# Performance work log

Hardware: AMD Instinct MI355X
Metric: run time of the kernel (lower is better)

The kernel has to match this reference:

```python
import jax, jax.numpy as jnp
import numpy as np

N_NODES = 20000
N_EDGES = 320000
N_ADJ = 4
D = 256
CSTR = [0, 1]          # constrained adjacency subset for the last step
RATIO = 1.0
LN_EPS = 1e-5


def setup_inputs() -> dict:
    key = jax.random.key(0)
    ks = jax.random.split(key, 10)
    x = jax.random.normal(ks[0], (N_NODES, D), dtype=jnp.float32)
    rows = jax.random.randint(ks[1], (N_ADJ, N_EDGES), 0, N_NODES)
    cols = jax.random.randint(ks[2], (N_ADJ, N_EDGES), 0, N_NODES)
    vals = jax.random.uniform(ks[3], (N_ADJ, N_EDGES), dtype=jnp.float32)
    W = jax.random.normal(ks[4], (D, D), dtype=jnp.float32) * (1.0 / np.sqrt(D))
    b = jax.random.normal(ks[5], (D,), dtype=jnp.float32) * 0.02
    ws_seq_0 = jax.random.uniform(ks[6], (2, N_ADJ - 1), dtype=jnp.float32)
    ws_seq_1 = jax.random.uniform(ks[7], (len(CSTR),), dtype=jnp.float32)
    ws_res_0 = jax.random.uniform(ks[8], (1, N_ADJ), dtype=jnp.float32)
    ws_res_1 = jax.random.uniform(ks[9], (2, len(CSTR) + 1), dtype=jnp.float32)
    return {"x": x, "rows": rows, "cols": cols, "vals": vals, "W": W, "b": b,
            "ws_seq_0": ws_seq_0, "ws_seq_1": ws_seq_1,
            "ws_res_0": ws_res_0, "ws_res_1": ws_res_1}


def reference(x, rows, cols, vals, W, b, ws_seq_0, ws_seq_1, ws_res_0, ws_res_1):
    n_nodes = x.shape[0]

    def spmm(a, h):
        # sparse [n,n] @ h : gather source features, scale, scatter-add by row
        return jax.ops.segment_sum(vals[a][:, None] * h[cols[a]], rows[a],
                                   num_segments=n_nodes)

    def op(h, adj_ids, w):
        # Op with k=1: random.sample selects ALL operators -> weighted mean
        acc = w[0] * spmm(adj_ids[0], h)
        for j, a in enumerate(adj_ids[1:], start=1):
            acc = acc + w[j] * spmm(a, h)
        return acc / len(adj_ids)

    h = x @ W + b                      # affine: [n_nodes, D]
    states = [h]
    # step i=0: seq only (res sum over states[:0] is empty -> 0), edge == 1
    s1 = op(states[0], [0, 1, 2], ws_seq_0[0])          # adjs[:-1]
    states.append(s1)
    # step i=1: seq on states[1] over adjs[:-1], res on states[0] over all adjs
    s2 = op(states[1], [0, 1, 2], ws_seq_0[1]) + RATIO * op(states[0], [0, 1, 2, 3], ws_res_0[0])
    states.append(s2)
    # last step: cstr adjacencies for seq; cstr + last adj for residuals
    out_seq = op(states[2], CSTR, ws_seq_1)
    res_ids = CSTR + [N_ADJ - 1]
    out_res = op(states[0], res_ids, ws_res_1[0]) + op(states[1], res_ids, ws_res_1[1])
    out = out_seq + RATIO * out_res
    # LayerNorm without affine params
    mu = jnp.mean(out, axis=-1, keepdims=True)
    var = jnp.var(out, axis=-1, keepdims=True)
    out = (out - mu) * jax.lax.rsqrt(var + LN_EPS)
    return jax.nn.gelu(out, approximate=False)
```

## Files before the change

### kernel.cpp

```cpp
#include <hip/hip_runtime.h>
#include <hip/hip_bf16.h>

#define N_NODES 20000
#define N_EDGES 320000
#define N_ADJ   4
#define D       256
#define DH      128
#define RPA     20004

#define NBUCK   79
#define NGRP    40
#define EPB     8000
#define GCAP    192
#define BMAX    4736
#define MMBLK   1250

typedef __attribute__((ext_vector_type(8))) short bf8;
typedef __attribute__((ext_vector_type(4))) float f4;


__device__ __forceinline__ unsigned f2bf_bits(float x) {
    unsigned u = __float_as_uint(x);
    return (u + 0x7FFFu + ((u >> 16) & 1u)) >> 16;
}
__device__ __forceinline__ unsigned pack_bf2(float lo, float hi) {
    return f2bf_bits(lo) | (f2bf_bits(hi) << 16);
}
__device__ __forceinline__ float bf_lo(unsigned p) { return __uint_as_float(p << 16); }
__device__ __forceinline__ float bf_hi(unsigned p) { return __uint_as_float(p & 0xFFFF0000u); }


__global__ __launch_bounds__(1024) void prep_kernel(const int* __restrict__ rows,
                                                    const int* __restrict__ cols,
                                                    const float* __restrict__ vals,
                                                    int* __restrict__ cnt,
                                                    uint2* __restrict__ stage,
                                                    const float* __restrict__ W,
                                                    uint4* __restrict__ wh,
                                                    uint4* __restrict__ wl) {
    __shared__ int lcnt[NBUCK];
    int g = blockIdx.x, a = blockIdx.y, t = threadIdx.x;

    if (g >= NGRP) {
        if (a != 0) return;
        for (int i = (g - NGRP) * 1024 + t; i < 8192; i += 2048) {
            int lane = i & 63;
            int tile = i >> 6;
            int ks = tile >> 4, n = tile & 15;
            int m = lane & 15, quad = lane >> 4;
            int col = n * 16 + m;
            int k0  = ks * 32 + quad * 8;
            unsigned hbits[8], lbits[8];
            #pragma unroll
            for (int j = 0; j < 8; ++j) {
                float v = W[(k0 + j) * D + col];
                unsigned hb = f2bf_bits(v);
                float lo = v - __uint_as_float(hb << 16);
                hbits[j] = hb;
                lbits[j] = f2bf_bits(lo);
            }
            uint4 hh, ll;
            hh.x = hbits[0] | (hbits[1] << 16); hh.y = hbits[2] | (hbits[3] << 16);
            hh.z = hbits[4] | (hbits[5] << 16); hh.w = hbits[6] | (hbits[7] << 16);
            ll.x = lbits[0] | (lbits[1] << 16); ll.y = lbits[2] | (lbits[3] << 16);
            ll.z = lbits[4] | (lbits[5] << 16); ll.w = lbits[6] | (lbits[7] << 16);
            wh[i] = hh;
            wl[i] = ll;
        }
        return;
    }

    if (t < NBUCK) lcnt[t] = 0;
    __syncthreads();
    int e0 = g * EPB;
    #pragma unroll 1
    for (int i = 0; i < EPB; i += 1024) {
        int e = e0 + i + t;
        if (i + t < EPB) {
            int r   = rows[a * N_EDGES + e];
            int c   = cols[a * N_EDGES + e];
            float v = vals[a * N_EDGES + e];
            int b   = r >> 8;
            int idx = atomicAdd(&lcnt[b], 1);
            if (idx < GCAP) {
                stage[(size_t)((a * NBUCK + b) * NGRP + g) * GCAP + idx] =
                    make_uint2((f2bf_bits(v) << 16) | (unsigned)c, (unsigned)(r & 255));
            }
        }
    }
    __syncthreads();
    if (t < NBUCK) cnt[(a * NBUCK + t) * NGRP + g] = min(lcnt[t], GCAP);
}


__global__ __launch_bounds__(256) void mm_kernel(const float* __restrict__ x,
                                                 const uint4* __restrict__ wh,
                                                 const uint4* __restrict__ wl,
                                                 const float* __restrict__ bvec,
                                                 unsigned* __restrict__ hp) {
    int t = threadIdx.x;
    int wid = t >> 6, lane = t & 63;
    int r0 = blockIdx.x * 16;
    int m = lane & 15, quad = lane >> 4;

    const float* xr = x + (size_t)(r0 + m) * D + quad * 8;
    bf8 ah[8], al[8];
    #pragma unroll
    for (int ks = 0; ks < 8; ++ks) {
        float4 v0 = *(const float4*)(xr + ks * 32);
        float4 v1 = *(const float4*)(xr + ks * 32 + 4);
        float xs[8] = {v0.x, v0.y, v0.z, v0.w, v1.x, v1.y, v1.z, v1.w};
        #pragma unroll
        for (int j = 0; j < 8; ++j) {
            unsigned hb = f2bf_bits(xs[j]);
            float lo = xs[j] - __uint_as_float(hb << 16);
            ah[ks][j] = (short)hb;
            al[ks][j] = (short)f2bf_bits(lo);
        }
    }

    #pragma unroll
    for (int i = 0; i < 4; ++i) {
        int n = wid * 4 + i;
        f4 c = {0.f, 0.f, 0.f, 0.f};
        #pragma unroll
        for (int ks = 0; ks < 8; ++ks) {
            uint4 bh4 = wh[(ks * 16 + n) * 64 + lane];
            uint4 bl4 = wl[(ks * 16 + n) * 64 + lane];
            bf8 bh = *(bf8*)&bh4;
            bf8 bl = *(bf8*)&bl4;
            c = __builtin_amdgcn_mfma_f32_16x16x32_bf16(ah[ks], bh, c, 0, 0, 0);
            c = __builtin_amdgcn_mfma_f32_16x16x32_bf16(al[ks], bh, c, 0, 0, 0);
            c = __builtin_amdgcn_mfma_f32_16x16x32_bf16(ah[ks], bl, c, 0, 0, 0);
        }
        int col = n * 16 + m;
        float bb = bvec[col];
        #pragma unroll
        for (int reg = 0; reg < 4; ++reg) {
            float v = c[reg] + bb;
            float o = __shfl_xor(v, 1, 64);
            if ((m & 1) == 0) {
                hp[(r0 + quad * 4 + reg) * DH + (col >> 1)] = pack_bf2(v, o);
            }
        }
    }
}


__global__ __launch_bounds__(256) void bsort_kernel(const int* __restrict__ cnt,
                                                    const uint2* __restrict__ stage,
                                                    unsigned* __restrict__ csr,
                                                    int* __restrict__ row_ptr) {
    __shared__ uint2 recs[BMAX];
    __shared__ int scn[256];
    __shared__ int offs[256];
    __shared__ int gbase_s;
    int t = threadIdx.x;

    int linear = blockIdx.x;
    int a = linear / NBUCK, b = linear % NBUCK;

    if (t == 0) gbase_s = 0;
    __syncthreads();
    int part = 0;
    for (int i = t; i < b * NGRP; i += 256) part += cnt[a * (NBUCK * NGRP) + i];
    #pragma unroll
    for (int off = 32; off > 0; off >>= 1) part += __shfl_xor(part, off, 64);
    if ((t & 63) == 0) atomicAdd(&gbase_s, part);

    int goff = 0;
    #pragma unroll 1
    for (int g = 0; g < NGRP; ++g) {
        int c = cnt[(a * NBUCK + b) * NGRP + g];
        const uint2* src = stage + (size_t)((a * NBUCK + b) * NGRP + g) * GCAP;
        for (int i = t; i < c; i += 256) {
            int d = goff + i;
            if (d < BMAX) recs[d] = src[i];
        }
        goff += c;
    }
    int total = min(goff, BMAX);

    scn[t] = 0;
    offs[t] = 0;
    __syncthreads();
    for (int i = t; i < total; i += 256) atomicAdd(&scn[recs[i].y], 1);
    __syncthreads();
    int mycnt = scn[t];
    for (int off = 1; off < 256; off <<= 1) {
        int add = (t >= off) ? scn[t - off] : 0;
        __syncthreads();
        scn[t] += add;
        __syncthreads();
    }
    int excl = scn[t] - mycnt;
    __syncthreads();
    scn[t] = excl;
    __syncthreads();

    int gbase = gbase_s;
    for (int i = t; i < total; i += 256) {
        int lr  = recs[i].y;
        int pos = scn[lr] + atomicAdd(&offs[lr], 1);
        csr[(size_t)a * N_EDGES + gbase + pos] = recs[i].x;
    }
    int r = b * 256 + t;
    if (r <= N_NODES) row_ptr[(size_t)a * RPA + r] = gbase + excl;
}


__device__ __forceinline__ void gather_seg(const unsigned* __restrict__ E, int beg, int end,
                                           const uint2* __restrict__ feat2, int lane,
                                           float* __restrict__ s ) {
    int n = end - beg;
    const unsigned* e = E + beg;
    int m8 = n & ~7;
    if (m8) {
        unsigned rec[8];
        #pragma unroll
        for (int j = 0; j < 8; ++j) rec[j] = e[j];
        for (int i = 8; ; i += 8) {
            uint2 p[8];
            #pragma unroll
            for (int j = 0; j < 8; ++j)
                p[j] = feat2[((rec[j] & 0xFFFFu) << 6) + lane];
            bool more = i < m8;
            unsigned nrec[8];
            if (more) {
                #pragma unroll
                for (int j = 0; j < 8; ++j) nrec[j] = e[i + j];
            }
            #pragma unroll
            for (int j = 0; j < 8; ++j) {
                float v = __uint_as_float(rec[j] & 0xFFFF0000u);
                s[0] += v * bf_lo(p[j].x);
                s[1] += v * bf_hi(p[j].x);
                s[2] += v * bf_lo(p[j].y);
                s[3] += v * bf_hi(p[j].y);
            }
            if (!more) break;
            #pragma unroll
            for (int j = 0; j < 8; ++j) rec[j] = nrec[j];
        }
    }
    for (int i = m8; i < n; ++i) {
        unsigned rr = e[i];
        uint2 pp = feat2[((rr & 0xFFFFu) << 6) + lane];
        float vv = __uint_as_float(rr & 0xFFFF0000u);
        s[0] += vv * bf_lo(pp.x);
        s[1] += vv * bf_hi(pp.x);
        s[2] += vv * bf_lo(pp.y);
        s[3] += vv * bf_hi(pp.y);
    }
}


__global__ __launch_bounds__(256) void stage1_kernel(const uint2* __restrict__ hp2,
                                                     const int* __restrict__ row_ptr,
                                                     const unsigned* __restrict__ csr,
                                                     const float* __restrict__ wseq0,
                                                     const float* __restrict__ wres0,
                                                     const float* __restrict__ wres1,
                                                     uint2* __restrict__ s1p2,
                                                     uint2* __restrict__ s2p2,
                                                     float4* __restrict__ outp4) {
    int t = threadIdx.x, wid = t >> 6, lane = t & 63;
    int r = blockIdx.x * 4 + wid;
    float acc[N_ADJ][4];
    #pragma unroll
    for (int a = 0; a < N_ADJ; ++a) {
        acc[a][0] = acc[a][1] = acc[a][2] = acc[a][3] = 0.f;
        const int* rp = row_ptr + (size_t)a * RPA;
        int beg = __builtin_amdgcn_readfirstlane(rp[r]);
        int end = __builtin_amdgcn_readfirstlane(rp[r + 1]);
        gather_seg(csr + (size_t)a * N_EDGES, beg, end, hp2, lane, acc[a]);
    }
    const float third = 1.f / 3.f;
    float w0 = wseq0[0] * third, w1 = wseq0[1] * third, w2 = wseq0[2] * third;
    float q0 = wres0[0] * 0.25f, q1 = wres0[1] * 0.25f, q2 = wres0[2] * 0.25f, q3 = wres0[3] * 0.25f;
    float u0 = wres1[0] * third, u1 = wres1[1] * third, u2 = wres1[2] * third;
    float s1v[4], s2v[4], ov[4];
    #pragma unroll
    for (int j = 0; j < 4; ++j) {
        s1v[j] = w0 * acc[0][j] + w1 * acc[1][j] + w2 * acc[2][j];
        s2v[j] = q0 * acc[0][j] + q1 * acc[1][j] + q2 * acc[2][j] + q3 * acc[3][j];
        ov[j]  = u0 * acc[0][j] + u1 * acc[1][j] + u2 * acc[3][j];
    }
    int o = r * 64 + lane;
    s1p2[o]  = make_uint2(pack_bf2(s1v[0], s1v[1]), pack_bf2(s1v[2], s1v[3]));
    s2p2[o]  = make_uint2(pack_bf2(s2v[0], s2v[1]), pack_bf2(s2v[2], s2v[3]));
    outp4[o] = make_float4(ov[0], ov[1], ov[2], ov[3]);
}


__global__ __launch_bounds__(256) void stage2_kernel(const uint2* __restrict__ s1p2,
                                                     const int* __restrict__ row_ptr,
                                                     const unsigned* __restrict__ csr,
                                                     const float* __restrict__ wseq0,
                                                     const float* __restrict__ wres1,
                                                     uint2* __restrict__ s2p2,
                                                     float4* __restrict__ outp4) {
    int t = threadIdx.x, wid = t >> 6, lane = t & 63;
    int r = blockIdx.x * 4 + wid;
    float acc[N_ADJ][4];
    #pragma unroll
    for (int a = 0; a < N_ADJ; ++a) {
        acc[a][0] = acc[a][1] = acc[a][2] = acc[a][3] = 0.f;
        const int* rp = row_ptr + (size_t)a * RPA;
        int beg = __builtin_amdgcn_readfirstlane(rp[r]);
        int end = __builtin_amdgcn_readfirstlane(rp[r + 1]);
        gather_seg(csr + (size_t)a * N_EDGES, beg, end, s1p2, lane, acc[a]);
    }
    const float third = 1.f / 3.f;
    float w3 = wseq0[3] * third, w4 = wseq0[4] * third, w5 = wseq0[5] * third;
    float u3 = wres1[3] * third, u4 = wres1[4] * third, u5 = wres1[5] * third;
    int o = r * 64 + lane;
    uint2 sp = s2p2[o];
    float c0 = bf_lo(sp.x) + w3 * acc[0][0] + w4 * acc[1][0] + w5 * acc[2][0];
    float c1 = bf_hi(sp.x) + w3 * acc[0][1] + w4 * acc[1][1] + w5 * acc[2][1];
    float c2 = bf_lo(sp.y) + w3 * acc[0][2] + w4 * acc[1][2] + w5 * acc[2][2];
    float c3 = bf_hi(sp.y) + w3 * acc[0][3] + w4 * acc[1][3] + w5 * acc[2][3];
    s2p2[o] = make_uint2(pack_bf2(c0, c1), pack_bf2(c2, c3));
    float4 op = outp4[o];
    op.x += u3 * acc[0][0] + u4 * acc[1][0] + u5 * acc[3][0];
    op.y += u3 * acc[0][1] + u4 * acc[1][1] + u5 * acc[3][1];
    op.z += u3 * acc[0][2] + u4 * acc[1][2] + u5 * acc[3][2];
    op.w += u3 * acc[0][3] + u4 * acc[1][3] + u5 * acc[3][3];
    outp4[o] = op;
}


__global__ __launch_bounds__(256) void stage3_kernel(const uint2* __restrict__ s2p2,
                                                     const int* __restrict__ row_ptr,
                                                     const unsigned* __restrict__ csr,
                                                     const float* __restrict__ wseq1,
                                                     float4* __restrict__ outp4) {
    int t = threadIdx.x, wid = t >> 6, lane = t & 63;
    int r = blockIdx.x * 4 + wid;
    float acc[2][4];
    #pragma unroll
    for (int a = 0; a < 2; ++a) {
        acc[a][0] = acc[a][1] = acc[a][2] = acc[a][3] = 0.f;
        const int* rp = row_ptr + (size_t)a * RPA;
        int beg = __builtin_amdgcn_readfirstlane(rp[r]);
        int end = __builtin_amdgcn_readfirstlane(rp[r + 1]);
        gather_seg(csr + (size_t)a * N_EDGES, beg, end, s2p2, lane, acc[a]);
    }
    float e0 = wseq1[0] * 0.5f, e1 = wseq1[1] * 0.5f;
    int o = r * 64 + lane;
    float4 op = outp4[o];
    float v0 = op.x + e0 * acc[0][0] + e1 * acc[1][0];
    float v1 = op.y + e0 * acc[0][1] + e1 * acc[1][1];
    float v2 = op.z + e0 * acc[0][2] + e1 * acc[1][2];
    float v3 = op.w + e0 * acc[0][3] + e1 * acc[1][3];

    float sv = v0 + v1 + v2 + v3;
    float sq = v0 * v0 + v1 * v1 + v2 * v2 + v3 * v3;
    #pragma unroll
    for (int off = 32; off > 0; off >>= 1) {
        sv += __shfl_xor(sv, off, 64);
        sq += __shfl_xor(sq, off, 64);
    }
    float mu   = sv * (1.f / 256.f);
    float var  = sq * (1.f / 256.f) - mu * mu;
    float rstd = rsqrtf(var + 1e-5f);
    float y0 = (v0 - mu) * rstd;
    float y1 = (v1 - mu) * rstd;
    float y2 = (v2 - mu) * rstd;
    float y3 = (v3 - mu) * rstd;
    const float is2 = 0.70710678118654752440f;
    outp4[o] = make_float4(0.5f * y0 * (1.f + erff(y0 * is2)),
                           0.5f * y1 * (1.f + erff(y1 * is2)),
                           0.5f * y2 * (1.f + erff(y2 * is2)),
                           0.5f * y3 * (1.f + erff(y3 * is2)));
}


extern "C" void kernel_launch(void* const* d_in, const int* in_sizes, int n_in,
                              void* d_out, int out_size, void* d_ws, size_t ws_size,
                              hipStream_t stream) {
    const float* x     = (const float*)d_in[0];
    const int*   rows  = (const int*)d_in[1];
    const int*   cols  = (const int*)d_in[2];
    const float* vals  = (const float*)d_in[3];
    const float* W     = (const float*)d_in[4];
    const float* b     = (const float*)d_in[5];
    const float* wseq0 = (const float*)d_in[6];
    const float* wseq1 = (const float*)d_in[7];
    const float* wres0 = (const float*)d_in[8];
    const float* wres1 = (const float*)d_in[9];
    float4* outp4 = (float4*)d_out;

    char* p = (char*)d_ws;
    unsigned* hp  = (unsigned*)p; p += (size_t)N_NODES * DH * 4;
    unsigned* s1p = (unsigned*)p; p += (size_t)N_NODES * DH * 4;
    unsigned* s2p = (unsigned*)p; p += (size_t)N_NODES * DH * 4;
    int* row_ptr  = (int*)p;      p += (size_t)N_ADJ * RPA * 4;
    int* cnt      = (int*)p;      p += (N_ADJ * NBUCK * NGRP * 4 + 127) / 128 * 128;
    uint4* wh     = (uint4*)p;    p += 8192 * 16;
    uint4* wl     = (uint4*)p;    p += 8192 * 16;
    unsigned* csr = (unsigned*)p;
    uint2* stage  = (uint2*)s1p;

    prep_kernel<<<dim3(NGRP + 2, N_ADJ), 1024, 0, stream>>>(rows, cols, vals, cnt,
                                                            stage, W, wh, wl);
    mm_kernel<<<MMBLK, 256, 0, stream>>>(x, wh, wl, b, hp);
    bsort_kernel<<<NBUCK * N_ADJ, 256, 0, stream>>>(cnt, stage, csr, row_ptr);

    stage1_kernel<<<N_NODES / 4, 256, 0, stream>>>((const uint2*)hp, row_ptr, csr,
                                                   wseq0, wres0, wres1,
                                                   (uint2*)s1p, (uint2*)s2p, outp4);
    stage2_kernel<<<N_NODES / 4, 256, 0, stream>>>((const uint2*)s1p, row_ptr, csr,
                                                   wseq0, wres1, (uint2*)s2p, outp4);
    stage3_kernel<<<N_NODES / 4, 256, 0, stream>>>((const uint2*)s2p, row_ptr, csr,
                                                   wseq1, outp4);
}
```

Measured before the change: 331.7 us.

## Replace bucketed staging sort with global-atomic histogram, scan, and scatter CSR build

Swaps the two-pass bucket staging and in-LDS sort used to build the per-adjacency CSR for a counting sort: a memset, a global-atomic row histogram, a single-block-per-adjacency prefix scan, and an atomic scatter into CSR slots. This drops the staging buffer, the capacity caps and the per-bucket LDS sort, at the cost of more global atomics and an extra kernel launch. Edge order within a row becomes nondeterministic, which can change the floating-point summation order.

```diff
diff --git a/kernel.cpp b/kernel.cpp
--- a/kernel.cpp
+++ b/kernel.cpp
@@ -8,11 +8,8 @@
 #define DH      128
 #define RPA     20004
 
-#define NBUCK   79
-#define NGRP    40
-#define EPB     8000
-#define GCAP    192
-#define BMAX    4736
+#define HB      160
+#define EPB2    2000
 #define MMBLK   1250
 
 typedef __attribute__((ext_vector_type(8))) short bf8;
@@ -30,20 +27,16 @@
 __device__ __forceinline__ float bf_hi(unsigned p) { return __uint_as_float(p & 0xFFFF0000u); }
 
 
-__global__ __launch_bounds__(1024) void prep_kernel(const int* __restrict__ rows,
-                                                    const int* __restrict__ cols,
-                                                    const float* __restrict__ vals,
+__global__ __launch_bounds__(1024) void hist_kernel(const int* __restrict__ rows,
                                                     int* __restrict__ cnt,
-                                                    uint2* __restrict__ stage,
                                                     const float* __restrict__ W,
                                                     uint4* __restrict__ wh,
                                                     uint4* __restrict__ wl) {
-    __shared__ int lcnt[NBUCK];
     int g = blockIdx.x, a = blockIdx.y, t = threadIdx.x;
 
-    if (g >= NGRP) {
+    if (g >= HB) {
         if (a != 0) return;
-        for (int i = (g - NGRP) * 1024 + t; i < 8192; i += 2048) {
+        for (int i = (g - HB) * 1024 + t; i < 8192; i += 2048) {
             int lane = i & 63;
             int tile = i >> 6;
             int ks = tile >> 4, n = tile & 15;
@@ -70,26 +63,67 @@
         return;
     }
 
-    if (t < NBUCK) lcnt[t] = 0;
+    int e0 = a * N_EDGES + g * EPB2;
+    for (int i = t; i < EPB2; i += 1024) {
+        int r = rows[e0 + i];
+        atomicAdd(&cnt[a * N_NODES + r], 1);
+    }
+}
+
+
+__global__ __launch_bounds__(1024) void scan_kernel(int* __restrict__ cnt,
+                                                    int* __restrict__ row_ptr) {
+    __shared__ int ts[1024];
+    int a = blockIdx.x, t = threadIdx.x;
+    int base = t * 20;
+    int* ca = cnt + a * N_NODES;
+    int loc[20];
+    int sum = 0;
+    #pragma unroll
+    for (int j = 0; j < 20; ++j) {
+        int r = base + j;
+        int v = (r < N_NODES) ? ca[r] : 0;
+        loc[j] = sum;
+        sum += v;
+    }
+    ts[t] = sum;
     __syncthreads();
-    int e0 = g * EPB;
-    #pragma unroll 1
-    for (int i = 0; i < EPB; i += 1024) {
-        int e = e0 + i + t;
-        if (i + t < EPB) {
-            int r   = rows[a * N_EDGES + e];
-            int c   = cols[a * N_EDGES + e];
-            float v = vals[a * N_EDGES + e];
-            int b   = r >> 8;
-            int idx = atomicAdd(&lcnt[b], 1);
-            if (idx < GCAP) {
-                stage[(size_t)((a * NBUCK + b) * NGRP + g) * GCAP + idx] =
-                    make_uint2((f2bf_bits(v) << 16) | (unsigned)c, (unsigned)(r & 255));
-            }
-        }
-    }
-    __syncthreads();
-    if (t < NBUCK) cnt[(a * NBUCK + t) * NGRP + g] = min(lcnt[t], GCAP);
+    for (int off = 1; off < 1024; off <<= 1) {
+        int add = (t >= off) ? ts[t - off] : 0;
+        __syncthreads();
+        ts[t] += add;
+        __syncthreads();
+    }
+    int excl = ts[t] - sum;
+    int* rp = row_ptr + (size_t)a * RPA;
+    #pragma unroll
+    for (int j = 0; j < 20; ++j) {
+        int r = base + j;
+        if (r < N_NODES) {
+            int bofs = excl + loc[j];
+            rp[r] = bofs;
+            ca[r] = bofs;
+        }
+    }
+    if (t == 0) rp[N_NODES] = N_EDGES;
+}
+
+
+__global__ __launch_bounds__(1024) void scatter_kernel(const int* __restrict__ rows,
+                                                       const int* __restrict__ cols,
+                                                       const float* __restrict__ vals,
+                                                       int* __restrict__ cnt,
+                                                       unsigned* __restrict__ csr) {
+    int g = blockIdx.x, a = blockIdx.y, t = threadIdx.x;
+    int e0 = a * N_EDGES + g * EPB2;
+    for (int i = t; i < EPB2; i += 1024) {
+        int e = e0 + i;
+        int r   = rows[e];
+        int c   = cols[e];
+        float v = vals[e];
+        int pos = atomicAdd(&cnt[a * N_NODES + r], 1);
+        csr[(size_t)a * N_EDGES + pos] = (f2bf_bits(v) << 16) | (unsigned)c;
+    }
 }
 
 
@@ -144,68 +178,6 @@
             }
         }
     }
-}
-
-
-__global__ __launch_bounds__(256) void bsort_kernel(const int* __restrict__ cnt,
-                                                    const uint2* __restrict__ stage,
-                                                    unsigned* __restrict__ csr,
-                                                    int* __restrict__ row_ptr) {
-    __shared__ uint2 recs[BMAX];
-    __shared__ int scn[256];
-    __shared__ int offs[256];
-    __shared__ int gbase_s;
-    int t = threadIdx.x;
-
-    int linear = blockIdx.x;
-    int a = linear / NBUCK, b = linear % NBUCK;
-
-    if (t == 0) gbase_s = 0;
-    __syncthreads();
-    int part = 0;
-    for (int i = t; i < b * NGRP; i += 256) part += cnt[a * (NBUCK * NGRP) + i];
-    #pragma unroll
-    for (int off = 32; off > 0; off >>= 1) part += __shfl_xor(part, off, 64);
-    if ((t & 63) == 0) atomicAdd(&gbase_s, part);
-
-    int goff = 0;
-    #pragma unroll 1
-    for (int g = 0; g < NGRP; ++g) {
-        int c = cnt[(a * NBUCK + b) * NGRP + g];
-        const uint2* src = stage + (size_t)((a * NBUCK + b) * NGRP + g) * GCAP;
-        for (int i = t; i < c; i += 256) {
-            int d = goff + i;
-            if (d < BMAX) recs[d] = src[i];
-        }
-        goff += c;
-    }
-    int total = min(goff, BMAX);
-
-    scn[t] = 0;
-    offs[t] = 0;
-    __syncthreads();
-    for (int i = t; i < total; i += 256) atomicAdd(&scn[recs[i].y], 1);
-    __syncthreads();
-    int mycnt = scn[t];
-    for (int off = 1; off < 256; off <<= 1) {
-        int add = (t >= off) ? scn[t - off] : 0;
-        __syncthreads();
-        scn[t] += add;
-        __syncthreads();
-    }
-    int excl = scn[t] - mycnt;
-    __syncthreads();
-    scn[t] = excl;
-    __syncthreads();
-
-    int gbase = gbase_s;
-    for (int i = t; i < total; i += 256) {
-        int lr  = recs[i].y;
-        int pos = scn[lr] + atomicAdd(&offs[lr], 1);
-        csr[(size_t)a * N_EDGES + gbase + pos] = recs[i].x;
-    }
-    int r = b * 256 + t;
-    if (r <= N_NODES) row_ptr[(size_t)a * RPA + r] = gbase + excl;
 }
 
 
@@ -396,16 +368,16 @@
     unsigned* s1p = (unsigned*)p; p += (size_t)N_NODES * DH * 4;
     unsigned* s2p = (unsigned*)p; p += (size_t)N_NODES * DH * 4;
     int* row_ptr  = (int*)p;      p += (size_t)N_ADJ * RPA * 4;
-    int* cnt      = (int*)p;      p += (N_ADJ * NBUCK * NGRP * 4 + 127) / 128 * 128;
     uint4* wh     = (uint4*)p;    p += 8192 * 16;
     uint4* wl     = (uint4*)p;    p += 8192 * 16;
     unsigned* csr = (unsigned*)p;
-    uint2* stage  = (uint2*)s1p;
-
-    prep_kernel<<<dim3(NGRP + 2, N_ADJ), 1024, 0, stream>>>(rows, cols, vals, cnt,
-                                                            stage, W, wh, wl);
+    int* cnt = (int*)s1p;
+
+    hipMemsetAsync(cnt, 0, (size_t)N_ADJ * N_NODES * 4, stream);
+    hist_kernel<<<dim3(HB + 2, N_ADJ), 1024, 0, stream>>>(rows, cnt, W, wh, wl);
+    scan_kernel<<<N_ADJ, 1024, 0, stream>>>(cnt, row_ptr);
+    scatter_kernel<<<dim3(HB, N_ADJ), 1024, 0, stream>>>(rows, cols, vals, cnt, csr);
     mm_kernel<<<MMBLK, 256, 0, stream>>>(x, wh, wl, b, hp);
-    bsort_kernel<<<NBUCK * N_ADJ, 256, 0, stream>>>(cnt, stage, csr, row_ptr);
 
     stage1_kernel<<<N_NODES / 4, 256, 0, stream>>>((const uint2*)hp, row_ptr, csr,
                                                    wseq0, wres0, wres1,
```

Result: slower. 453.4 us (+36.7%).

## Use finer 64-row sort buckets and sort CSR before the matmul

Applied to the files above, without the earlier changes.

Row buckets shrink from 256 rows to 64 rows, so there are 313 buckets with a per-group capacity of 72. The bucket-sort kernel drops its large shared-memory record buffer and reads the staged records from global memory twice, once to count and once to scatter. Launching about four times as many lighter blocks is meant to raise occupancy and parallelism in CSR construction. The staging buffer now overlaps the hp feature buffer, so bsort must run before mm_kernel, which the launch order now does. The costs are the repeated global reads and a longer cnt prefix scan per block.

```diff
diff --git a/kernel.cpp b/kernel.cpp
--- a/kernel.cpp
+++ b/kernel.cpp
@@ -8,11 +8,10 @@
 #define DH      128
 #define RPA     20004
 
-#define NBUCK   79
+#define NBUCK   313
 #define NGRP    40
 #define EPB     8000
-#define GCAP    192
-#define BMAX    4736
+#define GCAP    72
 #define MMBLK   1250
 
 typedef __attribute__((ext_vector_type(8))) short bf8;
@@ -80,16 +79,75 @@
             int r   = rows[a * N_EDGES + e];
             int c   = cols[a * N_EDGES + e];
             float v = vals[a * N_EDGES + e];
-            int b   = r >> 8;
+            int b   = r >> 6;
             int idx = atomicAdd(&lcnt[b], 1);
             if (idx < GCAP) {
                 stage[(size_t)((a * NBUCK + b) * NGRP + g) * GCAP + idx] =
-                    make_uint2((f2bf_bits(v) << 16) | (unsigned)c, (unsigned)(r & 255));
+                    make_uint2((f2bf_bits(v) << 16) | (unsigned)c, (unsigned)(r & 63));
             }
         }
     }
     __syncthreads();
     if (t < NBUCK) cnt[(a * NBUCK + t) * NGRP + g] = min(lcnt[t], GCAP);
+}
+
+
+__global__ __launch_bounds__(256) void bsort_kernel(const int* __restrict__ cnt,
+                                                    const uint2* __restrict__ stage,
+                                                    unsigned* __restrict__ csr,
+                                                    int* __restrict__ row_ptr) {
+    __shared__ int scn[64];
+    __shared__ int offs[64];
+    __shared__ int gbase_s;
+    int t = threadIdx.x;
+
+    int linear = blockIdx.x;
+    int a = linear / NBUCK, b = linear % NBUCK;
+
+    if (t == 0) gbase_s = 0;
+    if (t < 64) { scn[t] = 0; offs[t] = 0; }
+    __syncthreads();
+
+    int part = 0;
+    for (int i = t; i < b * NGRP; i += 256) part += cnt[a * (NBUCK * NGRP) + i];
+    #pragma unroll
+    for (int off = 32; off > 0; off >>= 1) part += __shfl_xor(part, off, 64);
+    if ((t & 63) == 0) atomicAdd(&gbase_s, part);
+
+    const int* cb = cnt + (size_t)(a * NBUCK + b) * NGRP;
+    #pragma unroll 1
+    for (int g = 0; g < NGRP; ++g) {
+        int c = cb[g];
+        const uint2* src = stage + (size_t)((a * NBUCK + b) * NGRP + g) * GCAP;
+        for (int i = t; i < c; i += 256) atomicAdd(&scn[src[i].y], 1);
+    }
+    __syncthreads();
+
+    int mycnt = (t < 64) ? scn[t] : 0;
+    for (int off = 1; off < 64; off <<= 1) {
+        int add = (t >= off && t < 64) ? scn[t - off] : 0;
+        __syncthreads();
+        if (t < 64) scn[t] += add;
+        __syncthreads();
+    }
+    int excl = (t < 64) ? scn[t] - mycnt : 0;
+    __syncthreads();
+    if (t < 64) scn[t] = excl;
+    __syncthreads();
+
+    int gbase = gbase_s;
+    #pragma unroll 1
+    for (int g = 0; g < NGRP; ++g) {
+        int c = cb[g];
+        const uint2* src = stage + (size_t)((a * NBUCK + b) * NGRP + g) * GCAP;
+        for (int i = t; i < c; i += 256) {
+            uint2 rec = src[i];
+            int pos = scn[rec.y] + atomicAdd(&offs[rec.y], 1);
+            csr[(size_t)a * N_EDGES + gbase + pos] = rec.x;
+        }
+    }
+    int r = b * 64 + t;
+    if (t < 64 && r <= N_NODES) row_ptr[(size_t)a * RPA + r] = gbase + excl;
 }
 
 
@@ -144,68 +202,6 @@
             }
         }
     }
-}
-
-
-__global__ __launch_bounds__(256) void bsort_kernel(const int* __restrict__ cnt,
-                                                    const uint2* __restrict__ stage,
-                                                    unsigned* __restrict__ csr,
-                                                    int* __restrict__ row_ptr) {
-    __shared__ uint2 recs[BMAX];
-    __shared__ int scn[256];
-    __shared__ int offs[256];
-    __shared__ int gbase_s;
-    int t = threadIdx.x;
-
-    int linear = blockIdx.x;
-    int a = linear / NBUCK, b = linear % NBUCK;
-
-    if (t == 0) gbase_s = 0;
-    __syncthreads();
-    int part = 0;
-    for (int i = t; i < b * NGRP; i += 256) part += cnt[a * (NBUCK * NGRP) + i];
-    #pragma unroll
-    for (int off = 32; off > 0; off >>= 1) part += __shfl_xor(part, off, 64);
-    if ((t & 63) == 0) atomicAdd(&gbase_s, part);
-
-    int goff = 0;
-    #pragma unroll 1
-    for (int g = 0; g < NGRP; ++g) {
-        int c = cnt[(a * NBUCK + b) * NGRP + g];
-        const uint2* src = stage + (size_t)((a * NBUCK + b) * NGRP + g) * GCAP;
-        for (int i = t; i < c; i += 256) {
-            int d = goff + i;
-            if (d < BMAX) recs[d] = src[i];
-        }
-        goff += c;
-    }
-    int total = min(goff, BMAX);
-
-    scn[t] = 0;
-    offs[t] = 0;
-    __syncthreads();
-    for (int i = t; i < total; i += 256) atomicAdd(&scn[recs[i].y], 1);
-    __syncthreads();
-    int mycnt = scn[t];
-    for (int off = 1; off < 256; off <<= 1) {
-        int add = (t >= off) ? scn[t - off] : 0;
-        __syncthreads();
-        scn[t] += add;
-        __syncthreads();
-    }
-    int excl = scn[t] - mycnt;
-    __syncthreads();
-    scn[t] = excl;
-    __syncthreads();
-
-    int gbase = gbase_s;
-    for (int i = t; i < total; i += 256) {
-        int lr  = recs[i].y;
-        int pos = scn[lr] + atomicAdd(&offs[lr], 1);
-        csr[(size_t)a * N_EDGES + gbase + pos] = recs[i].x;
-    }
-    int r = b * 256 + t;
-    if (r <= N_NODES) row_ptr[(size_t)a * RPA + r] = gbase + excl;
 }
 
 
@@ -396,16 +392,16 @@
     unsigned* s1p = (unsigned*)p; p += (size_t)N_NODES * DH * 4;
     unsigned* s2p = (unsigned*)p; p += (size_t)N_NODES * DH * 4;
     int* row_ptr  = (int*)p;      p += (size_t)N_ADJ * RPA * 4;
-    int* cnt      = (int*)p;      p += (N_ADJ * NBUCK * NGRP * 4 + 127) / 128 * 128;
+    int* cnt      = (int*)p;      p += ((size_t)N_ADJ * NBUCK * NGRP * 4 + 127) / 128 * 128;
     uint4* wh     = (uint4*)p;    p += 8192 * 16;
     uint4* wl     = (uint4*)p;    p += 8192 * 16;
     unsigned* csr = (unsigned*)p;
-    uint2* stage  = (uint2*)s1p;
+    uint2* stage  = (uint2*)hp;
 
     prep_kernel<<<dim3(NGRP + 2, N_ADJ), 1024, 0, stream>>>(rows, cols, vals, cnt,
                                                             stage, W, wh, wl);
+    bsort_kernel<<<NBUCK * N_ADJ, 256, 0, stream>>>(cnt, stage, csr, row_ptr);
     mm_kernel<<<MMBLK, 256, 0, stream>>>(x, wh, wl, b, hp);
-    bsort_kernel<<<NBUCK * N_ADJ, 256, 0, stream>>>(cnt, stage, csr, row_ptr);
 
     stage1_kernel<<<N_NODES / 4, 256, 0, stream>>>((const uint2*)hp, row_ptr, csr,
                                                    wseq0, wres0, wres1,
```

Result: no change. 337.7 us (+1.8%).
